# Kernel optimization log

Measured on AMD Instinct MI355X. Metric: run time of the kernel, lower is better.

The kernel has to match this reference:

```python
import jax, jax.numpy as jnp
import numpy as np

ALPHA = -100.0


def setup_inputs() -> dict:
    key = jax.random.key(0)
    k1, k2 = jax.random.split(key)
    input_seqs = jax.random.normal(k1, (512, 1024), dtype=jnp.float32)
    shapelets = jax.random.normal(k2, (100, 50), dtype=jnp.float32)
    return {"input_seqs": input_seqs, "shapelets": shapelets}


def reference(input_seqs, shapelets):
    """Sliding-window squared distance + softmin-weighted pooling.

    input_seqs: (n, Q) float
    shapelets : (K, L) float
    returns   : (n, K) float  -- softmin-pooled normalized sq. distance
    """
    n, Q = input_seqs.shape
    K, L = shapelets.shape
    J = Q - L  # original code uses Q - L (not Q - L + 1); kept faithful

    # ||x[j:j+L]||^2 for every window via cumulative sums (no explicit loop)
    csum = jnp.concatenate(
        [jnp.zeros((n, 1), input_seqs.dtype), jnp.cumsum(input_seqs * input_seqs, axis=1)],
        axis=1,
    )  # (n, Q+1)
    sq_win = csum[:, L:L + J] - csum[:, :J]  # (n, J)

    # cross term x[j:j+L] . s_k via windowed gather + small GEMM
    idx = jnp.arange(J)[:, None] + jnp.arange(L)[None, :]  # (J, L)
    windows = input_seqs[:, idx]  # (n, J, L)
    cross = jnp.einsum("njl,kl->njk", windows, shapelets)  # (n, J, K)

    s_sq = jnp.sum(shapelets * shapelets, axis=1)  # (K,)

    # D[i, j, k] = ||x_i[j:j+L] - s_k||^2 / L
    D = (sq_win[:, :, None] - 2.0 * cross + s_sq[None, None, :]) / L  # (n, J, K)

    # subtract per-(i,k) min over window positions (as in the original)
    Dm = D - jnp.min(D, axis=1, keepdims=True)

    # softmin-weighted average: sum_j Dm * exp(alpha*Dm) / sum_j exp(alpha*Dm)
    w = jnp.exp(ALPHA * Dm)  # stable: alpha<0 and Dm>=0 after min-shift
    M = jnp.sum(Dm * w, axis=1) / jnp.sum(w, axis=1)  # (n, K)
    return M
```

## Files before the change

### kernel.cpp

```cpp
#include <hip/hip_runtime.h>


#define N_SEQ   512
#define Q_LEN   1024
#define K_SH    100
#define L_SH    50
#define J_WIN   974
#define NTILE   7
#define MTILES  61
#define RINV_L  0.02f
#define PAD_SQ  4e31f
#define CQ      (-2.8853900817779268f)

#define CPR     1064

typedef short  short8 __attribute__((ext_vector_type(8)));
typedef float  f32x4  __attribute__((ext_vector_type(4)));
typedef unsigned int uintx4 __attribute__((ext_vector_type(4)));

union V8 { short8 s; uintx4 u; };

__device__ __forceinline__ unsigned int bf16h(float f) {
    unsigned int b = __float_as_uint(f);
    return (b + 0x7FFFu + ((b >> 16) & 1u)) >> 16;
}
__device__ __forceinline__ float bf16back(unsigned int h) {
    return __uint_as_float(h << 16);
}

__global__ __launch_bounds__(448, 2)
void softmin_mfma_kernel(const float* __restrict__ x,
                         const float* __restrict__ sh,
                         float* __restrict__ out) {
    __shared__ __align__(16) short cp[16 * CPR];
    __shared__ __align__(16) float lds_xf[1056];
    __shared__ __align__(16) float lds_sqw[984];

    const int i    = blockIdx.x;
    const int tid  = threadIdx.x;
    const int lane = tid & 63;
    const int w    = tid >> 6;
    const int g    = lane >> 4;
    const int bcol = lane & 15;

    short8 bh0, bh1, blo0, blo1;
    {
        const int n = w * 16 + bcol;
        float sv[16];
        #pragma unroll
        for (int e = 0; e < 16; ++e) sv[e] = 0.f;
        if (n < K_SH) {
            const float* srow = sh + n * L_SH;
            const float2* p0 = (const float2*)(srow + 8 * g);
            #pragma unroll
            for (int q = 0; q < 4; ++q) { float2 v = p0[q]; sv[2*q] = v.x; sv[2*q+1] = v.y; }
            if (g < 2) {
                const float2* p1 = (const float2*)(srow + 32 + 8 * g);
                #pragma unroll
                for (int q = 0; q < 4; ++q) { float2 v = p1[q]; sv[8+2*q] = v.x; sv[9+2*q] = v.y; }
            } else if (g == 2) {
                float2 v = *(const float2*)(srow + 48);
                sv[8] = v.x; sv[9] = v.y;
            }
        }
        unsigned int hb[16], lb[16];
        #pragma unroll
        for (int e = 0; e < 16; ++e) {
            hb[e] = bf16h(sv[e]);
            lb[e] = bf16h(sv[e] - bf16back(hb[e]));
        }
        V8 a, b, c, d;
        a.u = uintx4{hb[0]|(hb[1]<<16),  hb[2]|(hb[3]<<16),  hb[4]|(hb[5]<<16),  hb[6]|(hb[7]<<16)};
        b.u = uintx4{hb[8]|(hb[9]<<16),  hb[10]|(hb[11]<<16),hb[12]|(hb[13]<<16),hb[14]|(hb[15]<<16)};
        c.u = uintx4{lb[0]|(lb[1]<<16),  lb[2]|(lb[3]<<16),  lb[4]|(lb[5]<<16),  lb[6]|(lb[7]<<16)};
        d.u = uintx4{lb[8]|(lb[9]<<16),  lb[10]|(lb[11]<<16),lb[12]|(lb[13]<<16),lb[14]|(lb[15]<<16)};
        bh0 = a.s; bh1 = b.s; blo0 = c.s; blo1 = d.s;
    }

    {
        const float4* gx = (const float4*)(x + (size_t)i * Q_LEN);
        float4* lx = (float4*)lds_xf;
        if (tid < 256) lx[tid] = gx[tid];
        if (tid < 8)   lx[256 + tid] = make_float4(0.f, 0.f, 0.f, 0.f);
    }
    __syncthreads();

    if (tid < 246) {
        const float4* xf4 = (const float4*)lds_xf;
        float r0, r1, r2, r3;
        if (tid < 244) {
            float v[56];
            #pragma unroll
            for (int q = 0; q < 14; ++q) {
                float4 a = xf4[tid + q];
                v[4*q] = a.x; v[4*q+1] = a.y; v[4*q+2] = a.z; v[4*q+3] = a.w;
            }
            float s0 = 0.f;
            #pragma unroll
            for (int l = 0; l < L_SH; ++l) s0 = fmaf(v[l], v[l], s0);
            float s1 = fmaf(v[50], v[50], s0 - v[0]*v[0]);
            float s2 = fmaf(v[51], v[51], s1 - v[1]*v[1]);
            float s3 = fmaf(v[52], v[52], s2 - v[2]*v[2]);
            r0 = s0; r1 = s1; r2 = s2; r3 = s3;
            if (4*tid + 2 >= J_WIN) r2 = PAD_SQ;
            if (4*tid + 3 >= J_WIN) r3 = PAD_SQ;
        } else {
            r0 = r1 = r2 = r3 = PAD_SQ;
        }
        *(float4*)&lds_sqw[4*tid] = make_float4(r0, r1, r2, r3);
    }

    if (tid < 132) {
        const float4* xf4 = (const float4*)lds_xf;
        float4 a = xf4[2*tid], b = xf4[2*tid + 1];
        float xv[8] = {a.x, a.y, a.z, a.w, b.x, b.y, b.z, b.w};
        unsigned int hh[8], rr[8];
        #pragma unroll
        for (int e = 0; e < 8; ++e) {
            hh[e] = bf16h(xv[e]);
            rr[e] = bf16h(xv[e] - bf16back(hh[e]));
        }
        *(uintx4*)&cp[8*tid] =
            uintx4{hh[0]|(hh[1]<<16), hh[2]|(hh[3]<<16), hh[4]|(hh[5]<<16), hh[6]|(hh[7]<<16)};
        *(uintx4*)&cp[CPR + 8*tid] =
            uintx4{rr[0]|(rr[1]<<16), rr[2]|(rr[3]<<16), rr[4]|(rr[5]<<16), rr[6]|(rr[7]<<16)};
    }
    __syncthreads();

    if (tid < 262) {
        const int half = tid & 1, blk = tid >> 1;
        const uintx4 A  = *(const uintx4*)&cp[half*CPR + 8*blk];
        const uintx4 B4 = *(const uintx4*)&cp[half*CPR + 8*blk + 8];
        unsigned int s[8] = {A[0], A[1], A[2], A[3], B4[0], B4[1], B4[2], B4[3]};
        #pragma unroll
        for (int r = 1; r < 8; ++r) {
            const int p = r >> 1;
            unsigned int o[4];
            if ((r & 1) == 0) {
                #pragma unroll
                for (int e = 0; e < 4; ++e) o[e] = s[p + e];
            } else {
                #pragma unroll
                for (int e = 0; e < 4; ++e) o[e] = (s[p + e] >> 16) | (s[p + e + 1] << 16);
            }
            *(uintx4*)&cp[(2*r + half)*CPR + 8*blk] = uintx4{o[0], o[1], o[2], o[3]};
        }
    }
    __syncthreads();

    const int r7       = lane & 7;
    const int lane_off = 8 * ((lane >> 3) & 1) + 8 * g;
    const int abase0   = (2 * r7) * CPR + lane_off;

    float mreg = 1e30f;
    for (int mt = 0; mt < MTILES; ++mt) {
        const int j0 = mt << 4;
        const int ae = abase0 + j0;
        const short8 ah0 = *(const short8*)&cp[ae];
        const short8 ah1 = *(const short8*)&cp[ae + 32];
        const float4 sqv = *(const float4*)&lds_sqw[j0 + 4 * g];

        f32x4 a0 = {0.f, 0.f, 0.f, 0.f}, a1 = {0.f, 0.f, 0.f, 0.f};
        a0 = __builtin_amdgcn_mfma_f32_16x16x32_bf16(ah0, bh0, a0, 0, 0, 0);
        a1 = __builtin_amdgcn_mfma_f32_16x16x32_bf16(ah1, bh1, a1, 0, 0, 0);
        const float q0 = fmaf(a0[0], -2.f, fmaf(a1[0], -2.f, sqv.x));
        const float q1 = fmaf(a0[1], -2.f, fmaf(a1[1], -2.f, sqv.y));
        const float q2 = fmaf(a0[2], -2.f, fmaf(a1[2], -2.f, sqv.z));
        const float q3 = fmaf(a0[3], -2.f, fmaf(a1[3], -2.f, sqv.w));
        mreg = fminf(mreg, fminf(fminf(q0, q1), fminf(q2, q3)));
    }
    mreg = fminf(mreg, __shfl_xor(mreg, 16));
    mreg = fminf(mreg, __shfl_xor(mreg, 32));
    const float mq = mreg;

    float S = 0.f, T = 0.f, tmin = 1e30f;
    for (int mt = 0; mt < MTILES; ++mt) {
        const int j0 = mt << 4;
        const int ae = abase0 + j0;
        const short8 ah0 = *(const short8*)&cp[ae];
        const short8 ah1 = *(const short8*)&cp[ae + 32];
        const short8 al0 = *(const short8*)&cp[ae + CPR];
        const short8 al1 = *(const short8*)&cp[ae + CPR + 32];
        const float4 sqv = *(const float4*)&lds_sqw[j0 + 4 * g];

        f32x4 a0 = {0.f, 0.f, 0.f, 0.f}, a1 = {0.f, 0.f, 0.f, 0.f};
        a0 = __builtin_amdgcn_mfma_f32_16x16x32_bf16(ah0, bh0,  a0, 0, 0, 0);
        a1 = __builtin_amdgcn_mfma_f32_16x16x32_bf16(ah1, bh1,  a1, 0, 0, 0);
        a0 = __builtin_amdgcn_mfma_f32_16x16x32_bf16(al0, bh0,  a0, 0, 0, 0);
        a1 = __builtin_amdgcn_mfma_f32_16x16x32_bf16(al1, bh1,  a1, 0, 0, 0);
        a0 = __builtin_amdgcn_mfma_f32_16x16x32_bf16(ah0, blo0, a0, 0, 0, 0);
        a1 = __builtin_amdgcn_mfma_f32_16x16x32_bf16(ah1, blo1, a1, 0, 0, 0);

        const float t0 = fmaf(a0[0], -2.f, fmaf(a1[0], -2.f, sqv.x - mq));
        const float t1 = fmaf(a0[1], -2.f, fmaf(a1[1], -2.f, sqv.y - mq));
        const float t2 = fmaf(a0[2], -2.f, fmaf(a1[2], -2.f, sqv.z - mq));
        const float t3 = fmaf(a0[3], -2.f, fmaf(a1[3], -2.f, sqv.w - mq));
        tmin = fminf(tmin, fminf(fminf(t0, t1), fminf(t2, t3)));

        const float w0 = exp2f(t0 * CQ);
        const float w1 = exp2f(t1 * CQ);
        const float w2 = exp2f(t2 * CQ);
        const float w3 = exp2f(t3 * CQ);
        S += (w0 + w1) + (w2 + w3);
        float tv = T;
        tv = fmaf(t0, w0, tv);
        tv = fmaf(t1, w1, tv);
        tv = fmaf(t2, w2, tv);
        tv = fmaf(t3, w3, tv);
        T = tv;
    }

    tmin = fminf(tmin, __shfl_xor(tmin, 16));
    tmin = fminf(tmin, __shfl_xor(tmin, 32));
    S += __shfl_xor(S, 16);  S += __shfl_xor(S, 32);
    T += __shfl_xor(T, 16);  T += __shfl_xor(T, 32);

    if (lane < 16) {
        const int k = w * 16 + lane;
        if (k < K_SH) out[(size_t)i * K_SH + k] = (T / S - tmin) * RINV_L;
    }
}

extern "C" void kernel_launch(void* const* d_in, const int* in_sizes, int n_in,
                              void* d_out, int out_size, void* d_ws, size_t ws_size,
                              hipStream_t stream) {
    const float* x  = (const float*)d_in[0];
    const float* sh = (const float*)d_in[1];
    float* out = (float*)d_out;

    softmin_mfma_kernel<<<N_SEQ, 448, 0, stream>>>(x, sh, out);
}
```

Measured before the change: 94.40 us.

## Switch to 32x32x16 MFMA tiles and split window range across wave pairs

Replaces the 16x16x32 bf16 MFMA tiling (7 waves, one 16-shapelet column each) with 32x32x16 MFMA tiles over 4 shapelet column groups. The window dimension is split between two wave halves, giving 8 waves per block, and partial min/sum results are combined through shared memory. The aim is fewer MFMA issues and LDS A-fragment loads per output element, plus better MFMA throughput from larger tiles. In exchange it adds block-level syncs and LDS reductions, and the 16-element accumulators raise register pressure.

New measurement: 91.15 us. 1.04x faster.

```diff
diff --git a/kernel.cpp b/kernel.cpp
--- a/kernel.cpp
+++ b/kernel.cpp
@@ -6,8 +6,7 @@
 #define K_SH    100
 #define L_SH    50
 #define J_WIN   974
-#define NTILE   7
-#define MTILES  61
+#define MT32    31
 #define RINV_L  0.02f
 #define PAD_SQ  4e31f
 #define CQ      (-2.8853900817779268f)
@@ -15,7 +14,7 @@
 #define CPR     1064
 
 typedef short  short8 __attribute__((ext_vector_type(8)));
-typedef float  f32x4  __attribute__((ext_vector_type(4)));
+typedef float  f32x16 __attribute__((ext_vector_type(16)));
 typedef unsigned int uintx4 __attribute__((ext_vector_type(4)));
 
 union V8 { short8 s; uintx4 u; };
@@ -28,53 +27,58 @@
     return __uint_as_float(h << 16);
 }
 
-__global__ __launch_bounds__(448, 2)
+__global__ __launch_bounds__(512, 2)
 void softmin_mfma_kernel(const float* __restrict__ x,
                          const float* __restrict__ sh,
                          float* __restrict__ out) {
     __shared__ __align__(16) short cp[16 * CPR];
     __shared__ __align__(16) float lds_xf[1056];
-    __shared__ __align__(16) float lds_sqw[984];
+    __shared__ __align__(16) float lds_sqw[992];
+    __shared__ __align__(16) float gmT[256];
+    __shared__ __align__(16) float redM[256];
+    __shared__ __align__(16) float redS[256];
+    __shared__ __align__(16) float redT[256];
 
     const int i    = blockIdx.x;
     const int tid  = threadIdx.x;
     const int lane = tid & 63;
     const int w    = tid >> 6;
-    const int g    = lane >> 4;
-    const int bcol = lane & 15;
-
-    short8 bh0, bh1, blo0, blo1;
+    const int kt   = w & 3;
+    const int jh   = w >> 2;
+    const int col  = lane & 31;
+    const int hi   = lane >> 5;
+
+    short8 bh[4], bl[4];
     {
-        const int n = w * 16 + bcol;
-        float sv[16];
-        #pragma unroll
-        for (int e = 0; e < 16; ++e) sv[e] = 0.f;
-        if (n < K_SH) {
-            const float* srow = sh + n * L_SH;
-            const float2* p0 = (const float2*)(srow + 8 * g);
-            #pragma unroll
-            for (int q = 0; q < 4; ++q) { float2 v = p0[q]; sv[2*q] = v.x; sv[2*q+1] = v.y; }
-            if (g < 2) {
-                const float2* p1 = (const float2*)(srow + 32 + 8 * g);
+        const int n = kt * 32 + col;
+        const bool nok = (n < K_SH);
+        const float* srow = sh + (nok ? n : 0) * L_SH;
+        #pragma unroll
+        for (int km = 0; km < 4; ++km) {
+            const int k0 = 16 * km + 8 * hi;
+            float sv[8];
+            #pragma unroll
+            for (int e = 0; e < 8; ++e) sv[e] = 0.f;
+            if (nok) {
                 #pragma unroll
-                for (int q = 0; q < 4; ++q) { float2 v = p1[q]; sv[8+2*q] = v.x; sv[9+2*q] = v.y; }
-            } else if (g == 2) {
-                float2 v = *(const float2*)(srow + 48);
-                sv[8] = v.x; sv[9] = v.y;
-            }
-        }
-        unsigned int hb[16], lb[16];
-        #pragma unroll
-        for (int e = 0; e < 16; ++e) {
-            hb[e] = bf16h(sv[e]);
-            lb[e] = bf16h(sv[e] - bf16back(hb[e]));
-        }
-        V8 a, b, c, d;
-        a.u = uintx4{hb[0]|(hb[1]<<16),  hb[2]|(hb[3]<<16),  hb[4]|(hb[5]<<16),  hb[6]|(hb[7]<<16)};
-        b.u = uintx4{hb[8]|(hb[9]<<16),  hb[10]|(hb[11]<<16),hb[12]|(hb[13]<<16),hb[14]|(hb[15]<<16)};
-        c.u = uintx4{lb[0]|(lb[1]<<16),  lb[2]|(lb[3]<<16),  lb[4]|(lb[5]<<16),  lb[6]|(lb[7]<<16)};
-        d.u = uintx4{lb[8]|(lb[9]<<16),  lb[10]|(lb[11]<<16),lb[12]|(lb[13]<<16),lb[14]|(lb[15]<<16)};
-        bh0 = a.s; bh1 = b.s; blo0 = c.s; blo1 = d.s;
+                for (int e = 0; e < 8; e += 2) {
+                    if (k0 + e < L_SH) {
+                        float2 v = *(const float2*)(srow + k0 + e);
+                        sv[e] = v.x; sv[e + 1] = v.y;
+                    }
+                }
+            }
+            unsigned int hb[8], lb[8];
+            #pragma unroll
+            for (int e = 0; e < 8; ++e) {
+                hb[e] = bf16h(sv[e]);
+                lb[e] = bf16h(sv[e] - bf16back(hb[e]));
+            }
+            V8 H, Lo;
+            H.u  = uintx4{hb[0]|(hb[1]<<16), hb[2]|(hb[3]<<16), hb[4]|(hb[5]<<16), hb[6]|(hb[7]<<16)};
+            Lo.u = uintx4{lb[0]|(lb[1]<<16), lb[2]|(lb[3]<<16), lb[4]|(lb[5]<<16), lb[6]|(lb[7]<<16)};
+            bh[km] = H.s; bl[km] = Lo.s;
+        }
     }
 
     {
@@ -85,7 +89,7 @@
     }
     __syncthreads();
 
-    if (tid < 246) {
+    if (tid < 248) {
         const float4* xf4 = (const float4*)lds_xf;
         float r0, r1, r2, r3;
         if (tid < 244) {
@@ -149,75 +153,104 @@
     __syncthreads();
 
     const int r7       = lane & 7;
-    const int lane_off = 8 * ((lane >> 3) & 1) + 8 * g;
+    const int lane_off = 8 * ((lane >> 3) & 3) + 8 * hi;
     const int abase0   = (2 * r7) * CPR + lane_off;
 
     float mreg = 1e30f;
-    for (int mt = 0; mt < MTILES; ++mt) {
-        const int j0 = mt << 4;
-        const int ae = abase0 + j0;
-        const short8 ah0 = *(const short8*)&cp[ae];
-        const short8 ah1 = *(const short8*)&cp[ae + 32];
-        const float4 sqv = *(const float4*)&lds_sqw[j0 + 4 * g];
-
-        f32x4 a0 = {0.f, 0.f, 0.f, 0.f}, a1 = {0.f, 0.f, 0.f, 0.f};
-        a0 = __builtin_amdgcn_mfma_f32_16x16x32_bf16(ah0, bh0, a0, 0, 0, 0);
-        a1 = __builtin_amdgcn_mfma_f32_16x16x32_bf16(ah1, bh1, a1, 0, 0, 0);
-        const float q0 = fmaf(a0[0], -2.f, fmaf(a1[0], -2.f, sqv.x));
-        const float q1 = fmaf(a0[1], -2.f, fmaf(a1[1], -2.f, sqv.y));
-        const float q2 = fmaf(a0[2], -2.f, fmaf(a1[2], -2.f, sqv.z));
-        const float q3 = fmaf(a0[3], -2.f, fmaf(a1[3], -2.f, sqv.w));
-        mreg = fminf(mreg, fminf(fminf(q0, q1), fminf(q2, q3)));
-    }
-    mreg = fminf(mreg, __shfl_xor(mreg, 16));
+    for (int mt = jh; mt < MT32; mt += 2) {
+        const int j0 = mt << 5;
+        const int p  = abase0 + j0;
+        const short8 ah0 = *(const short8*)&cp[p];
+        const short8 ah1 = *(const short8*)&cp[p + 16];
+        const short8 ah2 = *(const short8*)&cp[p + 32];
+        const short8 ah3 = *(const short8*)&cp[p + 48];
+
+        f32x16 acc = {0.f,0.f,0.f,0.f,0.f,0.f,0.f,0.f,0.f,0.f,0.f,0.f,0.f,0.f,0.f,0.f};
+        acc = __builtin_amdgcn_mfma_f32_32x32x16_bf16(ah0, bh[0], acc, 0, 0, 0);
+        acc = __builtin_amdgcn_mfma_f32_32x32x16_bf16(ah1, bh[1], acc, 0, 0, 0);
+        acc = __builtin_amdgcn_mfma_f32_32x32x16_bf16(ah2, bh[2], acc, 0, 0, 0);
+        acc = __builtin_amdgcn_mfma_f32_32x32x16_bf16(ah3, bh[3], acc, 0, 0, 0);
+
+        #pragma unroll
+        for (int rg = 0; rg < 4; ++rg) {
+            const float4 sqv = *(const float4*)&lds_sqw[j0 + 8*rg + 4*hi];
+            const float q0 = fmaf(acc[4*rg+0], -2.f, sqv.x);
+            const float q1 = fmaf(acc[4*rg+1], -2.f, sqv.y);
+            const float q2 = fmaf(acc[4*rg+2], -2.f, sqv.z);
+            const float q3 = fmaf(acc[4*rg+3], -2.f, sqv.w);
+            mreg = fminf(mreg, fminf(fminf(q0, q1), fminf(q2, q3)));
+        }
+    }
     mreg = fminf(mreg, __shfl_xor(mreg, 32));
-    const float mq = mreg;
+    if (lane < 32) gmT[(jh * 4 + kt) * 32 + lane] = mreg;
+    __syncthreads();
+    const float mq = fminf(gmT[kt * 32 + col], gmT[128 + kt * 32 + col]);
 
     float S = 0.f, T = 0.f, tmin = 1e30f;
-    for (int mt = 0; mt < MTILES; ++mt) {
-        const int j0 = mt << 4;
-        const int ae = abase0 + j0;
-        const short8 ah0 = *(const short8*)&cp[ae];
-        const short8 ah1 = *(const short8*)&cp[ae + 32];
-        const short8 al0 = *(const short8*)&cp[ae + CPR];
-        const short8 al1 = *(const short8*)&cp[ae + CPR + 32];
-        const float4 sqv = *(const float4*)&lds_sqw[j0 + 4 * g];
-
-        f32x4 a0 = {0.f, 0.f, 0.f, 0.f}, a1 = {0.f, 0.f, 0.f, 0.f};
-        a0 = __builtin_amdgcn_mfma_f32_16x16x32_bf16(ah0, bh0,  a0, 0, 0, 0);
-        a1 = __builtin_amdgcn_mfma_f32_16x16x32_bf16(ah1, bh1,  a1, 0, 0, 0);
-        a0 = __builtin_amdgcn_mfma_f32_16x16x32_bf16(al0, bh0,  a0, 0, 0, 0);
-        a1 = __builtin_amdgcn_mfma_f32_16x16x32_bf16(al1, bh1,  a1, 0, 0, 0);
-        a0 = __builtin_amdgcn_mfma_f32_16x16x32_bf16(ah0, blo0, a0, 0, 0, 0);
-        a1 = __builtin_amdgcn_mfma_f32_16x16x32_bf16(ah1, blo1, a1, 0, 0, 0);
-
-        const float t0 = fmaf(a0[0], -2.f, fmaf(a1[0], -2.f, sqv.x - mq));
-        const float t1 = fmaf(a0[1], -2.f, fmaf(a1[1], -2.f, sqv.y - mq));
-        const float t2 = fmaf(a0[2], -2.f, fmaf(a1[2], -2.f, sqv.z - mq));
-        const float t3 = fmaf(a0[3], -2.f, fmaf(a1[3], -2.f, sqv.w - mq));
-        tmin = fminf(tmin, fminf(fminf(t0, t1), fminf(t2, t3)));
-
-        const float w0 = exp2f(t0 * CQ);
-        const float w1 = exp2f(t1 * CQ);
-        const float w2 = exp2f(t2 * CQ);
-        const float w3 = exp2f(t3 * CQ);
-        S += (w0 + w1) + (w2 + w3);
-        float tv = T;
-        tv = fmaf(t0, w0, tv);
-        tv = fmaf(t1, w1, tv);
-        tv = fmaf(t2, w2, tv);
-        tv = fmaf(t3, w3, tv);
-        T = tv;
-    }
-
-    tmin = fminf(tmin, __shfl_xor(tmin, 16));
+    for (int mt = jh; mt < MT32; mt += 2) {
+        const int j0 = mt << 5;
+        const int p  = abase0 + j0;
+        const short8 ah0 = *(const short8*)&cp[p];
+        const short8 ah1 = *(const short8*)&cp[p + 16];
+        const short8 ah2 = *(const short8*)&cp[p + 32];
+        const short8 ah3 = *(const short8*)&cp[p + 48];
+        const short8 al0 = *(const short8*)&cp[p + CPR];
+        const short8 al1 = *(const short8*)&cp[p + CPR + 16];
+        const short8 al2 = *(const short8*)&cp[p + CPR + 32];
+        const short8 al3 = *(const short8*)&cp[p + CPR + 48];
+
+        f32x16 acc = {0.f,0.f,0.f,0.f,0.f,0.f,0.f,0.f,0.f,0.f,0.f,0.f,0.f,0.f,0.f,0.f};
+        acc = __builtin_amdgcn_mfma_f32_32x32x16_bf16(ah0, bh[0], acc, 0, 0, 0);
+        acc = __builtin_amdgcn_mfma_f32_32x32x16_bf16(ah1, bh[1], acc, 0, 0, 0);
+        acc = __builtin_amdgcn_mfma_f32_32x32x16_bf16(ah2, bh[2], acc, 0, 0, 0);
+        acc = __builtin_amdgcn_mfma_f32_32x32x16_bf16(ah3, bh[3], acc, 0, 0, 0);
+        acc = __builtin_amdgcn_mfma_f32_32x32x16_bf16(al0, bh[0], acc, 0, 0, 0);
+        acc = __builtin_amdgcn_mfma_f32_32x32x16_bf16(al1, bh[1], acc, 0, 0, 0);
+        acc = __builtin_amdgcn_mfma_f32_32x32x16_bf16(al2, bh[2], acc, 0, 0, 0);
+        acc = __builtin_amdgcn_mfma_f32_32x32x16_bf16(al3, bh[3], acc, 0, 0, 0);
+        acc = __builtin_amdgcn_mfma_f32_32x32x16_bf16(ah0, bl[0], acc, 0, 0, 0);
+        acc = __builtin_amdgcn_mfma_f32_32x32x16_bf16(ah1, bl[1], acc, 0, 0, 0);
+        acc = __builtin_amdgcn_mfma_f32_32x32x16_bf16(ah2, bl[2], acc, 0, 0, 0);
+        acc = __builtin_amdgcn_mfma_f32_32x32x16_bf16(ah3, bl[3], acc, 0, 0, 0);
+
+        #pragma unroll
+        for (int rg = 0; rg < 4; ++rg) {
+            const float4 sqv = *(const float4*)&lds_sqw[j0 + 8*rg + 4*hi];
+            const float s0 = sqv.x - mq, s1 = sqv.y - mq;
+            const float s2 = sqv.z - mq, s3 = sqv.w - mq;
+            const float t0 = fmaf(acc[4*rg+0], -2.f, s0);
+            const float t1 = fmaf(acc[4*rg+1], -2.f, s1);
+            const float t2 = fmaf(acc[4*rg+2], -2.f, s2);
+            const float t3 = fmaf(acc[4*rg+3], -2.f, s3);
+            tmin = fminf(tmin, fminf(fminf(t0, t1), fminf(t2, t3)));
+            const float w0 = exp2f(t0 * CQ);
+            const float w1 = exp2f(t1 * CQ);
+            const float w2 = exp2f(t2 * CQ);
+            const float w3 = exp2f(t3 * CQ);
+            S += (w0 + w1) + (w2 + w3);
+            float tv = T;
+            tv = fmaf(t0, w0, tv);
+            tv = fmaf(t1, w1, tv);
+            tv = fmaf(t2, w2, tv);
+            tv = fmaf(t3, w3, tv);
+            T = tv;
+        }
+    }
+
     tmin = fminf(tmin, __shfl_xor(tmin, 32));
-    S += __shfl_xor(S, 16);  S += __shfl_xor(S, 32);
-    T += __shfl_xor(T, 16);  T += __shfl_xor(T, 32);
-
-    if (lane < 16) {
-        const int k = w * 16 + lane;
-        if (k < K_SH) out[(size_t)i * K_SH + k] = (T / S - tmin) * RINV_L;
+    S += __shfl_xor(S, 32);
+    T += __shfl_xor(T, 32);
+    if (lane < 32) {
+        const int idx = (jh * 4 + kt) * 32 + lane;
+        redM[idx] = tmin; redS[idx] = S; redT[idx] = T;
+    }
+    __syncthreads();
+
+    if (tid < 128) {
+        const float tm = fminf(redM[tid], redM[128 + tid]);
+        const float Sf = redS[tid] + redS[128 + tid];
+        const float Tf = redT[tid] + redT[128 + tid];
+        if (tid < K_SH) out[(size_t)i * K_SH + tid] = (Tf / Sf - tm) * RINV_L;
     }
 }
 
@@ -228,5 +261,5 @@
     const float* sh = (const float*)d_in[1];
     float* out = (float*)d_out;
 
-    softmin_mfma_kernel<<<N_SEQ, 448, 0, stream>>>(x, sh, out);
-}
+    softmin_mfma_kernel<<<N_SEQ, 512, 0, stream>>>(x, sh, out);
+}
```
